# Optimization experiments

Measured on AMD Instinct MI355X. Metric: run time of the kernel, lower is better.

## Reference

```python
import jax, jax.numpy as jnp
import numpy as np

B, C, H, W = 4, 768, 64, 64
NC_PRED = 200   # classes in preds/text (!= 171 to trigger retrieval path)
NC_MEM = 171    # memory/text_coco classes
TC = 256        # transform_channels
OC = 768        # out_channels
BN_EPS = 1e-5


def setup_inputs() -> dict:
    key = jax.random.key(0)
    ks = jax.random.split(key, 32)
    n = lambda k, s, sc=1.0: jax.random.normal(k, s, jnp.float32) * sc
    g = lambda k, c: 1.0 + 0.1 * jax.random.normal(k, (c,), jnp.float32)
    inp = {
        'feats': n(ks[0], (B, C, H, W)),
        'preds': n(ks[1], (B, NC_PRED, H, W)),
        'text': n(ks[2], (1, NC_PRED, 1, C)),
        'memory': n(ks[3], (NC_MEM, 1, C)),      # self.memory buffer
        'text_mem': n(ks[4], (NC_MEM, 1, C)),    # self.text buffer
        # query_project: two 1x1 conv + BN + ReLU
        'qw1': n(ks[5], (TC, C), C ** -0.5), 'qg1': g(ks[6], TC), 'qb1': n(ks[7], (TC,), 0.1),
        'qw2': n(ks[8], (TC, TC), TC ** -0.5), 'qg2': g(ks[9], TC), 'qb2': n(ks[10], (TC,), 0.1),
        # key_project: two 1x1 conv + BN + ReLU
        'kw1': n(ks[11], (TC, C), C ** -0.5), 'kg1': g(ks[12], TC), 'kb1': n(ks[13], (TC,), 0.1),
        'kw2': n(ks[14], (TC, TC), TC ** -0.5), 'kg2': g(ks[15], TC), 'kb2': n(ks[16], (TC,), 0.1),
        # value_project: 1x1 conv + BN + ReLU
        'vw': n(ks[17], (TC, C), C ** -0.5), 'vg': g(ks[18], TC), 'vb': n(ks[19], (TC,), 0.1),
        # out_project: 1x1 conv + BN + ReLU (TC -> C)
        'ow': n(ks[20], (C, TC), TC ** -0.5), 'og': g(ks[21], C), 'ob': n(ks[22], (C,), 0.1),
        # bottleneck: 3x3 conv (2C -> OC) + BN + ReLU
        'bw': n(ks[23], (OC, 2 * C, 3, 3), (2 * C * 9) ** -0.5), 'bg': g(ks[24], OC), 'bb': n(ks[25], (OC,), 0.1),
    }
    return inp


def _cbr(x, w, gamma, beta):
    # 1x1 conv (no bias) + eval-mode BN (mean=0, var=1) + ReLU
    y = jnp.einsum('oc,bchw->bohw', w, x)
    s = (gamma / jnp.sqrt(1.0 + BN_EPS))[None, :, None, None]
    return jax.nn.relu(y * s + beta[None, :, None, None])


def _forward(feats, preds, text, memory, text_mem,
             qw1, qg1, qb1, qw2, qg2, qb2,
             kw1, kg1, kb1, kw2, kg2, kb2,
             vw, vg, vb, ow, og, ob, bw, bg, bb):
    b, c, h, w = feats.shape
    nc = preds.shape[1]
    # softmax class weights per pixel: [B*H*W, NC]
    wcls = jax.nn.softmax(preds.transpose(0, 2, 3, 1).reshape(-1, nc), axis=-1)
    # --- retrieval: cosine sim + argmax + gather (nc != 171 branch) ---
    t = text[0, :, 0, :]          # [NC_PRED, C]
    tc = text_mem[:, 0, :]        # [NC_MEM, C]
    mem = memory[:, 0, :]         # [NC_MEM, C]
    den = jnp.linalg.norm(t, axis=1)[:, None] * jnp.linalg.norm(tc, axis=1)[None, :]
    sim = (t @ tc.T) / jnp.maximum(den, 1e-8)
    idx = jnp.argmax(sim, axis=1)            # [NC_PRED]
    D = mem[idx]                             # gathered memory rows [NC_PRED, C]
    # soft aggregation
    sel = (wcls @ D).reshape(b, h, w, c).transpose(0, 3, 1, 2)  # [B,C,H,W]
    # --- self-attention: query=feats, key/value=selected memory ---
    q = _cbr(_cbr(feats, qw1, qg1, qb1), qw2, qg2, qb2).reshape(b, TC, h * w).transpose(0, 2, 1)  # [B,HW,TC]
    k = _cbr(_cbr(sel, kw1, kg1, kb1), kw2, kg2, kb2).reshape(b, TC, h * w)                        # [B,TC,HW]
    v = _cbr(sel, vw, vg, vb).reshape(b, TC, h * w).transpose(0, 2, 1)                             # [B,HW,TC]
    att = jax.nn.softmax(jnp.einsum('bqc,bck->bqk', q, k) * (TC ** -0.5), axis=-1)                 # [B,HW,HW]
    ctx = jnp.einsum('bqk,bkc->bqc', att, v).transpose(0, 2, 1).reshape(b, TC, h, w)
    sel_out = _cbr(ctx, ow, og, ob)          # [B,C,H,W]
    # --- bottleneck: 3x3 conv + BN + ReLU on concat ---
    x = jnp.concatenate([feats, sel_out], axis=1)
    y = jax.lax.conv_general_dilated(x, bw, (1, 1), 'SAME',
                                     dimension_numbers=('NCHW', 'OIHW', 'NCHW'))
    s = (bg / jnp.sqrt(1.0 + BN_EPS))[None, :, None, None]
    return jax.nn.relu(y * s + bb[None, :, None, None])


def reference(feats, preds, text, memory, text_mem,
              qw1, qg1, qb1, qw2, qg2, qb2,
              kw1, kg1, kb1, kw2, kg2, kb2,
              vw, vg, vb, ow, og, ob, bw, bg, bb):
    return _forward(feats, preds, text, memory, text_mem,
                    qw1, qg1, qb1, qw2, qg2, qb2,
                    kw1, kg1, kb1, kw2, kg2, kb2,
                    vw, vg, vb, ow, og, ob, bw, bg, bb)
```

## Files before the change

### kernel.cpp

```cpp
#include <hip/hip_runtime.h>
#include <stdint.h>

typedef unsigned short u16;
typedef __attribute__((ext_vector_type(8))) short short8;
typedef __attribute__((ext_vector_type(4))) float f32x4;

#define RSQC 0.9999950000374997f
#define OUT_ELEMS 12582912

__device__ __forceinline__ float bf2f(u16 u) {
  union { uint32_t i; float f; } v; v.i = ((uint32_t)u) << 16; return v.f;
}
__device__ __forceinline__ u16 f2bf(float f) {
  union { uint32_t i; float f; } v; v.f = f;
  uint32_t i = v.i;
  i += 0x7fffu + ((i >> 16) & 1u);
  return (u16)(i >> 16);
}

__global__ __launch_bounds__(256) void probe_fill(float* out, float val) {
  for (size_t i = (size_t)blockIdx.x * 256 + threadIdx.x; i < OUT_ELEMS; i += (size_t)gridDim.x * 256)
    out[i] = val;
}


__global__ __launch_bounds__(64) void sim_argmax(const float* __restrict__ text,
                                                 const float* __restrict__ tmem,
                                                 int* __restrict__ idx) {
  const int i = blockIdx.x, lane = threadIdx.x;
  const float* t = text + (size_t)i * 768;
  float nt = 0.f;
  for (int c = lane; c < 768; c += 64) { float x = t[c]; nt += x * x; }
#pragma unroll
  for (int m = 32; m; m >>= 1) nt += __shfl_xor(nt, m);
  nt = sqrtf(nt);
  float best = -1e30f; int bj = 0x7fffffff;
  for (int j = lane; j < 171; j += 64) {
    const float* tc = tmem + (size_t)j * 768;
    float dot = 0.f, nc = 0.f;
    for (int c = 0; c < 768; ++c) {
      float y = tc[c];
      dot += t[c] * y;
      nc += y * y;
    }
    float den = fmaxf(nt * sqrtf(nc), 1e-8f);
    float s = dot / den;
    if (s > best || (s == best && j < bj)) { best = s; bj = j; }
  }
#pragma unroll
  for (int m = 32; m; m >>= 1) {
    float ob = __shfl_xor(best, m); int oj = __shfl_xor(bj, m);
    if (ob > best || (ob == best && oj < bj)) { best = ob; bj = oj; }
  }
  if (lane == 0) idx[i] = bj;
}

__global__ __launch_bounds__(256) void build_d(const float* __restrict__ memory,
                                               const int* __restrict__ idx,
                                               u16* __restrict__ D) {
  int i = blockIdx.x * 256 + threadIdx.x;
  if (i >= 256 * 768) return;
  int c = i % 768, j = i / 768;
  u16 v = 0;
  if (j < 200) {
    int ii = idx[j];
    ii = ii < 0 ? 0 : (ii > 170 ? 170 : ii);
    v = f2bf(memory[(size_t)ii * 768 + c]);
  }
  D[i] = v;
}

__global__ __launch_bounds__(256) void wcls_kernel(const float* __restrict__ preds,
                                                   u16* __restrict__ wcls) {
  const int pos = blockIdx.x * 256 + threadIdx.x;
  const int b = pos >> 12, hw = pos & 4095;
  const float* p = preds + (size_t)b * 200 * 4096 + hw;
  float mx = -1e30f;
  for (int n = 0; n < 200; ++n) mx = fmaxf(mx, p[(size_t)n * 4096]);
  float s = 0.f;
  for (int n = 0; n < 200; ++n) s += __expf(p[(size_t)n * 4096] - mx);
  const float inv = 1.f / s;
  u16* w = wcls + (size_t)pos * 256;
  for (int nc = 0; nc < 32; ++nc) {
    short8 v;
#pragma unroll
    for (int j = 0; j < 8; ++j) {
      int n = nc * 8 + j;
      float e = (n < 200) ? __expf(p[(size_t)n * 4096] - mx) * inv : 0.f;
      v[j] = (short)f2bf(e);
    }
    *(short8*)&w[nc * 8] = v;
  }
}

__global__ __launch_bounds__(256) void transpose_feats(const float* __restrict__ feats,
                                                       u16* __restrict__ ft) {
  __shared__ u16 t[64][65];
  const int bz = blockIdx.z, c0 = blockIdx.y * 64, p0 = blockIdx.x * 64;
  const int col = threadIdx.x & 63, row4 = threadIdx.x >> 6;
  const float* src = feats + ((size_t)bz * 768 + c0) * 4096 + p0;
#pragma unroll
  for (int i = 0; i < 16; ++i) {
    int ci = i * 4 + row4;
    t[ci][col] = f2bf(src[(size_t)ci * 4096 + col]);
  }
  __syncthreads();
  u16* dst = ft + ((size_t)bz * 4096 + p0) * 768 + c0;
#pragma unroll
  for (int i = 0; i < 16; ++i) {
    int pi = i * 4 + row4;
    dst[(size_t)pi * 768 + col] = t[col][pi];
  }
}

__global__ __launch_bounds__(256) void cast_w(const float* __restrict__ src,
                                              u16* __restrict__ dst, int n) {
  int i = blockIdx.x * 256 + threadIdx.x;
  if (i < n) dst[i] = f2bf(src[i]);
}

__global__ __launch_bounds__(256) void repack_frag(const float* __restrict__ bw,
                                                   u16* __restrict__ w9f, int c_base) {
  size_t i = (size_t)blockIdx.x * 256 + threadIdx.x;
  if (i >= (size_t)5308416) return;
  int j = (int)(i & 7);
  int lane = (int)((i >> 3) & 63);
  int rem = (int)(i >> 9);
  int mfrag = rem % 48;
  int pt = rem / 48;
  int tap = pt % 9;
  int kc = pt / 9;
  int o = mfrag * 16 + (lane & 15);
  int c = kc * 32 + (lane >> 4) * 8 + j;
  w9f[i] = f2bf(bw[((size_t)o * 1536 + c_base + c) * 9 + tap]);
}


template <bool EP>
__global__ __launch_bounds__(256) void gemm_std(
    const u16* __restrict__ A, const u16* __restrict__ Bt, u16* __restrict__ out,
    const float* __restrict__ g, const float* __restrict__ bia,
    int N, int K, int lda, int ldb) {
  __shared__ __attribute__((aligned(16))) u16 As[2][128 * 32];
  __shared__ __attribute__((aligned(16))) u16 Bs[2][128 * 32];
  const int tid = threadIdx.x, lane = tid & 63, wv = tid >> 6;
  const int wr = wv >> 1, wc = wv & 1;
  const int m0 = blockIdx.y * 128, n0 = blockIdx.x * 128;
  const int r0 = lane >> 2, ksl = (lane & 3) * 8;
  const int wofs = (lane >> 2) * 32 + (((lane & 3) ^ ((lane >> 3) & 3)) << 3);
  const int rsl = (((lane >> 4) ^ ((lane >> 1) & 3)) << 3);
  f32x4 acc[4][4] = {};
  const int nt = K >> 5;

  short8 a0[2], b0[2], a1[2], b1[2];
  auto LOAD = [&](int t, short8 av[2], short8 bv[2]) {
    const int k0 = t << 5;
#pragma unroll
    for (int i = 0; i < 2; ++i) {
      const int row = (wv * 2 + i) * 16 + r0;
      av[i] = *(const short8*)(A + (size_t)(m0 + row) * lda + k0 + ksl);
      bv[i] = *(const short8*)(Bt + (size_t)(n0 + row) * ldb + k0 + ksl);
    }
  };
  auto STORE = [&](int buf, short8 av[2], short8 bv[2]) {
#pragma unroll
    for (int i = 0; i < 2; ++i) {
      const int o = (wv * 2 + i) * 512 + wofs;
      *(short8*)&As[buf][o] = av[i];
      *(short8*)&Bs[buf][o] = bv[i];
    }
  };
  auto COMPUTE = [&](int buf) {
    short8 a[4], b[4];
#pragma unroll
    for (int mi = 0; mi < 4; ++mi)
      a[mi] = *(const short8*)&As[buf][(wr * 4 + mi) * 512 + (lane & 15) * 32 + rsl];
#pragma unroll
    for (int ni = 0; ni < 4; ++ni)
      b[ni] = *(const short8*)&Bs[buf][(wc * 4 + ni) * 512 + (lane & 15) * 32 + rsl];
#pragma unroll
    for (int mi = 0; mi < 4; ++mi)
#pragma unroll
      for (int ni = 0; ni < 4; ++ni)
        acc[mi][ni] = __builtin_amdgcn_mfma_f32_16x16x32_bf16(a[mi], b[ni], acc[mi][ni], 0, 0, 0);
  };

  LOAD(0, a0, b0);
  for (int t = 0; t < nt; t += 2) {
    STORE(0, a0, b0);
    __syncthreads();
    LOAD(t + 1, a1, b1);
    COMPUTE(0);
    STORE(1, a1, b1);
    __syncthreads();
    if (t + 2 < nt) LOAD(t + 2, a0, b0);
    COMPUTE(1);
  }
  const int mb = m0 + wr * 64 + ((lane >> 4) << 2);
  const int nb = n0 + wc * 64 + (lane & 15);
#pragma unroll
  for (int ni = 0; ni < 4; ++ni) {
    const int n = nb + ni * 16;
    float s = 1.f, bb_ = 0.f;
    if (EP) { s = g[n] * RSQC; bb_ = bia[n]; }
#pragma unroll
    for (int mi = 0; mi < 4; ++mi)
#pragma unroll
      for (int r = 0; r < 4; ++r) {
        float v = acc[mi][ni][r];
        if (EP) v = fmaxf(v * s + bb_, 0.f);
        out[(size_t)(mb + mi * 16 + r) * N + n] = f2bf(v);
      }
  }
}

__global__ __launch_bounds__(256) void gemm_swv(
    const u16* __restrict__ A, const u16* __restrict__ Bt, u16* __restrict__ out,
    const float* __restrict__ g, const float* __restrict__ bia,
    int Mtot, int K, int lda, int ldb) {
  __shared__ __attribute__((aligned(16))) u16 As[2][128 * 32];
  __shared__ __attribute__((aligned(16))) u16 Bs[2][128 * 32];
  const int tid = threadIdx.x, lane = tid & 63, wv = tid >> 6;
  const int wr = wv >> 1, wc = wv & 1;
  const int m0 = blockIdx.y * 128, n0 = blockIdx.x * 128;
  const int r0 = lane >> 2, ksl = (lane & 3) * 8;
  const int wofs = (lane >> 2) * 32 + (((lane & 3) ^ ((lane >> 3) & 3)) << 3);
  const int rsl = (((lane >> 4) ^ ((lane >> 1) & 3)) << 3);
  f32x4 acc[4][4] = {};
  const int nt = K >> 5;

  short8 a0[2], b0[2], a1[2], b1[2];
  auto LOAD = [&](int t, short8 av[2], short8 bv[2]) {
    const int k0 = t << 5;
#pragma unroll
    for (int i = 0; i < 2; ++i) {
      const int row = (wv * 2 + i) * 16 + r0;
      av[i] = *(const short8*)(A + (size_t)(m0 + row) * lda + k0 + ksl);
      bv[i] = *(const short8*)(Bt + (size_t)(n0 + row) * ldb + k0 + ksl);
    }
  };
  auto STORE = [&](int buf, short8 av[2], short8 bv[2]) {
#pragma unroll
    for (int i = 0; i < 2; ++i) {
      const int o = (wv * 2 + i) * 512 + wofs;
      *(short8*)&As[buf][o] = av[i];
      *(short8*)&Bs[buf][o] = bv[i];
    }
  };
  auto COMPUTE = [&](int buf) {
    short8 a[4], b[4];
#pragma unroll
    for (int mi = 0; mi < 4; ++mi)
      a[mi] = *(const short8*)&As[buf][(wr * 4 + mi) * 512 + (lane & 15) * 32 + rsl];
#pragma unroll
    for (int ni = 0; ni < 4; ++ni)
      b[ni] = *(const short8*)&Bs[buf][(wc * 4 + ni) * 512 + (lane & 15) * 32 + rsl];
#pragma unroll
    for (int mi = 0; mi < 4; ++mi)
#pragma unroll
      for (int ni = 0; ni < 4; ++ni)
        acc[mi][ni] = __builtin_amdgcn_mfma_f32_16x16x32_bf16(a[mi], b[ni], acc[mi][ni], 0, 0, 0);
  };

  LOAD(0, a0, b0);
  for (int t = 0; t < nt; t += 2) {
    STORE(0, a0, b0);
    __syncthreads();
    LOAD(t + 1, a1, b1);
    COMPUTE(0);
    STORE(1, a1, b1);
    __syncthreads();
    if (t + 2 < nt) LOAD(t + 2, a0, b0);
    COMPUTE(1);
  }
  const int mb = m0 + wr * 64 + ((lane >> 4) << 2);
  const int nb = n0 + wc * 64 + (lane & 15);
#pragma unroll
  for (int mi = 0; mi < 4; ++mi)
#pragma unroll
    for (int r = 0; r < 4; ++r) {
      const int m = mb + mi * 16 + r;
      const float s = g[m] * RSQC, bb_ = bia[m];
#pragma unroll
      for (int ni = 0; ni < 4; ++ni) {
        const int n = nb + ni * 16;
        out[((size_t)(n >> 12) * Mtot + m) * 4096 + (n & 4095)] =
            f2bf(fmaxf(acc[mi][ni][r] * s + bb_, 0.f));
      }
    }
}

template <int MODE>
__global__ __launch_bounds__(256) void conv_frag(
    const u16* __restrict__ Af, const u16* __restrict__ X, float* out,
    const float* __restrict__ g, const float* __restrict__ bia) {
  __shared__ __attribute__((aligned(16))) u16 Hb[264 * 32];
  const int tid = threadIdx.x, lane = tid & 63, wv = tid >> 6;
  const int wr = wv >> 1, wc = wv & 1;
  const int id = blockIdx.y * 128 + blockIdx.x;
  const int xcd = id & 7, sl = id >> 3;
  const int m0 = (sl % 6) * 128;
  const int n0 = (xcd * 16 + sl / 6) * 128;
  f32x4 acc[4][4] = {};

  int vmask[4];
#pragma unroll
  for (int i = 0; i < 4; ++i) {
    const int hw = (n0 + wc * 64 + i * 16 + (lane & 15)) & 4095;
    const int h = hw >> 6, w = hw & 63;
    int m = 0;
#pragma unroll
    for (int t = 0; t < 9; ++t)
      if ((unsigned)(h + t / 3 - 1) < 64u && (unsigned)(w + t % 3 - 1) < 64u) m |= 1 << t;
    vmask[i] = m;
  }

  const int fb = (m0 >> 4) + wr * 4;
  auto aload = [&](int kc, int tap, short8 d[4]) {
    const u16* base = Af + ((size_t)((kc * 9 + tap) * 48 + fb) << 9) + lane * 8;
#pragma unroll
    for (int mi = 0; mi < 4; ++mi) d[mi] = *(const short8*)(base + (mi << 9));
  };

  short8 acur[4], anxt[4];
  aload(0, 0, acur);
  for (int kc = 0; kc < 24; ++kc) {
    short8 hreg[5];
#pragma unroll
    for (int j = 0; j < 5; ++j) {
      const int cid = tid + j * 256;
      if (cid < 1032) {
        int q = n0 - 65 + (cid >> 2);
        q = q < 0 ? 0 : (q > 16383 ? 16383 : q);
        hreg[j] = *(const short8*)(X + (size_t)q * 768 + kc * 32 + (cid & 3) * 8);
      }
    }
    __syncthreads();
#pragma unroll
    for (int j = 0; j < 5; ++j) {
      const int cid = tid + j * 256;
      if (cid < 1032) {
        const int s = cid & 3, row = cid >> 2;
        *(short8*)((char*)Hb + row * 64 + ((s ^ ((row >> 1) & 3)) << 4)) = hreg[j];
      }
    }
    __syncthreads();
#pragma unroll
    for (int tap = 0; tap < 9; ++tap) {
      const int nk = (tap == 8) ? (kc == 23 ? 23 : kc + 1) : kc;
      const int ntp = (tap == 8) ? 0 : tap + 1;
      aload(nk, ntp, anxt);
      const int shift = (tap / 3 - 1) * 64 + (tap % 3 - 1);
#pragma unroll
      for (int ni = 0; ni < 4; ++ni) {
        const int hrow = wc * 64 + ni * 16 + (lane & 15) + 65 + shift;
        short8 bv = *(const short8*)((const char*)Hb + hrow * 64 +
                                     (((lane >> 4) ^ ((hrow >> 1) & 3)) << 4));
        short8 z = {};
        if (!((vmask[ni] >> tap) & 1)) bv = z;
#pragma unroll
        for (int mi = 0; mi < 4; ++mi)
          acc[mi][ni] = __builtin_amdgcn_mfma_f32_16x16x32_bf16(acur[mi], bv, acc[mi][ni], 0, 0, 0);
      }
#pragma unroll
      for (int mi = 0; mi < 4; ++mi) acur[mi] = anxt[mi];
    }
  }
  const int mb = m0 + wr * 64 + ((lane >> 4) << 2);
  const int nb = n0 + wc * 64 + (lane & 15);
#pragma unroll
  for (int mi = 0; mi < 4; ++mi)
#pragma unroll
    for (int r = 0; r < 4; ++r) {
      const int m = mb + mi * 16 + r;
      float s = 0.f, bb_ = 0.f;
      if (MODE == 2) { s = g[m] * RSQC; bb_ = bia[m]; }
#pragma unroll
      for (int ni = 0; ni < 4; ++ni) {
        const int n = nb + ni * 16;
        const size_t oidx = ((size_t)(n >> 12) * 768 + m) * 4096 + (n & 4095);
        if (MODE == 1) out[oidx] = acc[mi][ni][r];
        else out[oidx] = fmaxf((acc[mi][ni][r] + out[oidx]) * s + bb_, 0.f);
      }
    }
}

__global__ __launch_bounds__(256) void flash_attn(const u16* Q,
                                                  const u16* __restrict__ Kg,
                                                  const u16* __restrict__ Vt,
                                                  u16* ctx) {
  __shared__ __attribute__((aligned(16))) u16 KVs[64 * 256];
  __shared__ __attribute__((aligned(16))) u16 Ps[4096];
  const int tid = threadIdx.x, lane = tid & 63, wv = tid >> 6;
  const int b = blockIdx.y, q0 = blockIdx.x * 64;
  const u16* qb = Q + ((size_t)b * 4096 + q0) * 256;
  const u16* kb = Kg + (size_t)b * 4096 * 256;
  const u16* vb = Vt + (size_t)b * 256 * 4096;
  const float scale = 0.0625f;

  short8 qf[8];
  {
    const int arow = wv * 16 + (lane & 15);
    const u16* qrow = qb + (size_t)arow * 256 + (lane >> 4) * 8;
#pragma unroll
    for (int kk = 0; kk < 8; ++kk) qf[kk] = *(const short8*)(qrow + kk * 32);
  }
  float mreg[4] = {-1e30f, -1e30f, -1e30f, -1e30f};
  float lsum[4] = {0.f, 0.f, 0.f, 0.f};
  f32x4 o[16] = {};

  for (int t = 0; t < 64; ++t) {
    {
      const int r = tid >> 5, sb = (tid & 31) * 16;
      const char* ksrc = (const char*)(kb + (size_t)t * 64 * 256);
#pragma unroll
      for (int i = 0; i < 8; ++i) {
        int row = i * 8 + r;
        short8 v = *(const short8*)(ksrc + (size_t)row * 512 + sb);
        *(short8*)((char*)KVs + row * 512 + (sb ^ ((row & 7) << 4))) = v;
      }
    }
    __syncthreads();
    f32x4 s4[4] = {};
    __builtin_amdgcn_s_setprio(1);
#pragma unroll
    for (int kk = 0; kk < 8; ++kk) {
      const int cb = (kk * 32 + ((lane >> 4) * 8)) * 2;
#pragma unroll
      for (int ni = 0; ni < 4; ++ni) {
        const int brow = ni * 16 + (lane & 15);
        short8 bb = *(const short8*)((const char*)KVs + brow * 512 + (cb ^ ((brow & 7) << 4)));
        s4[ni] = __builtin_amdgcn_mfma_f32_16x16x32_bf16(qf[kk], bb, s4[ni], 0, 0, 0);
      }
    }
    __builtin_amdgcn_s_setprio(0);
    float al[4], p[4][4];
#pragma unroll
    for (int r = 0; r < 4; ++r) {
      float v0 = fmaxf(fmaxf(s4[0][r], s4[1][r]), fmaxf(s4[2][r], s4[3][r]));
      v0 = fmaxf(v0, __shfl_xor(v0, 1));
      v0 = fmaxf(v0, __shfl_xor(v0, 2));
      v0 = fmaxf(v0, __shfl_xor(v0, 4));
      v0 = fmaxf(v0, __shfl_xor(v0, 8));
      const float mn = fmaxf(mreg[r], v0 * scale);
      al[r] = __expf(mreg[r] - mn);
      mreg[r] = mn;
      float srow = 0.f;
#pragma unroll
      for (int ni = 0; ni < 4; ++ni) {
        float pv = __expf(s4[ni][r] * scale - mn);
        p[ni][r] = pv;
        srow += pv;
      }
      srow += __shfl_xor(srow, 1);
      srow += __shfl_xor(srow, 2);
      srow += __shfl_xor(srow, 4);
      srow += __shfl_xor(srow, 8);
      lsum[r] = lsum[r] * al[r] + srow;
    }
#pragma unroll
    for (int nf = 0; nf < 16; ++nf)
#pragma unroll
      for (int r = 0; r < 4; ++r) o[nf][r] *= al[r];
    {
      char* pbase = (char*)Ps + wv * 2048;
#pragma unroll
      for (int ni = 0; ni < 4; ++ni)
#pragma unroll
        for (int r = 0; r < 4; ++r) {
          const int row = ((lane >> 4) << 2) + r, col = ni * 16 + (lane & 15);
          *(u16*)(pbase + row * 128 + ((col * 2) ^ ((row & 7) << 4))) = f2bf(p[ni][r]);
        }
    }
    __syncthreads();
    {
      const int slot = tid & 7;
#pragma unroll
      for (int i = 0; i < 8; ++i) {
        const int cc = i * 32 + (tid >> 3);
        short8 v = *(const short8*)((const char*)vb + ((size_t)cc * 4096 + t * 64) * 2 + slot * 16);
        *(short8*)((char*)KVs + cc * 128 + ((slot * 16) ^ ((cc & 7) << 4))) = v;
      }
    }
    __syncthreads();
    short8 pa[2];
#pragma unroll
    for (int kk = 0; kk < 2; ++kk) {
      const int row = lane & 15;
      const int cb = (kk * 32 + ((lane >> 4) * 8)) * 2;
      pa[kk] = *(const short8*)((const char*)Ps + wv * 2048 + row * 128 + (cb ^ ((row & 7) << 4)));
    }
    __builtin_amdgcn_s_setprio(1);
#pragma unroll
    for (int nf = 0; nf < 16; ++nf) {
      const int crow = nf * 16 + (lane & 15);
#pragma unroll
      for (int kk = 0; kk < 2; ++kk) {
        const int kb2 = (kk * 32 + ((lane >> 4) * 8)) * 2;
        short8 bb = *(const short8*)((const char*)KVs + crow * 128 + (kb2 ^ ((crow & 7) << 4)));
        o[nf] = __builtin_amdgcn_mfma_f32_16x16x32_bf16(pa[kk], bb, o[nf], 0, 0, 0);
      }
    }
    __builtin_amdgcn_s_setprio(0);
    __syncthreads();
  }
  u16* cb_ = ctx + ((size_t)b * 4096 + q0) * 256;
#pragma unroll
  for (int r = 0; r < 4; ++r) {
    const int row = wv * 16 + ((lane >> 4) << 2) + r;
    const float inv = 1.f / lsum[r];
#pragma unroll
    for (int nf = 0; nf < 16; ++nf) {
      const int col = nf * 16 + (lane & 15);
      cb_[(size_t)row * 256 + col] = f2bf(o[nf][r] * inv);
    }
  }
}


extern "C" void kernel_launch(void* const* d_in, const int* in_sizes, int n_in,
                              void* d_out, int out_size, void* d_ws, size_t ws_size,
                              hipStream_t stream) {
  (void)in_sizes; (void)n_in; (void)out_size;
  const float* feats  = (const float*)d_in[0];
  const float* preds  = (const float*)d_in[1];
  const float* text   = (const float*)d_in[2];
  const float* memory = (const float*)d_in[3];
  const float* tmem   = (const float*)d_in[4];
  const float* qw1 = (const float*)d_in[5];  const float* qg1 = (const float*)d_in[6];  const float* qb1 = (const float*)d_in[7];
  const float* qw2 = (const float*)d_in[8];  const float* qg2 = (const float*)d_in[9];  const float* qb2 = (const float*)d_in[10];
  const float* kw1 = (const float*)d_in[11]; const float* kg1 = (const float*)d_in[12]; const float* kb1 = (const float*)d_in[13];
  const float* kw2 = (const float*)d_in[14]; const float* kg2 = (const float*)d_in[15]; const float* kb2 = (const float*)d_in[16];
  const float* vw  = (const float*)d_in[17]; const float* vg  = (const float*)d_in[18]; const float* vb  = (const float*)d_in[19];
  const float* ow  = (const float*)d_in[20]; const float* og  = (const float*)d_in[21]; const float* ob  = (const float*)d_in[22];
  const float* bw  = (const float*)d_in[23]; const float* bg  = (const float*)d_in[24]; const float* bb  = (const float*)d_in[25];

  float* dout = (float*)d_out;
  char* ws = (char*)d_ws;
  u16* featsT = (u16*)(ws);
  u16* selout = (u16*)(ws + 25165824);
  u16* S2     = (u16*)(ws + 50331648);
  u16* qw1c   = (u16*)(ws + 58720256);
  u16* kw1c   = (u16*)(ws + 59113472);
  u16* vwc    = (u16*)(ws + 59506688);
  u16* owc    = (u16*)(ws + 59899904);
  u16* qw2c   = (u16*)(ws + 60293120);
  u16* kw2c   = (u16*)(ws + 60424192);
  u16* w9     = S2;
  const size_t WS_NEED = 60948480;
  u16* D   = selout;
  u16* KD  = (u16*)((char*)selout + 393216);
  u16* VD  = (u16*)((char*)selout + 524288);
  int* idx = (int*)((char*)selout + 655360);
  u16* O0 = (u16*)dout;
  u16* O1 = O0 + 4194304;
  u16* O2 = O0 + 8388608;

  if (ws_size < WS_NEED) {
    probe_fill<<<2048, 256, 0, stream>>>(dout, 1000.0f);
    return;
  }

  u16* wcls = O0;
  u16* k1 = S2, *q1 = S2;
  u16* kbuf = O1, *vT = O2;
  u16* qbuf = O0, *ctx = O0;

  sim_argmax<<<200, 64, 0, stream>>>(text, tmem, idx);
  build_d<<<768, 256, 0, stream>>>(memory, idx, D);
  wcls_kernel<<<64, 256, 0, stream>>>(preds, wcls);
  transpose_feats<<<dim3(64, 12, 4), 256, 0, stream>>>(feats, featsT);
  cast_w<<<768, 256, 0, stream>>>(qw1, qw1c, 196608);
  cast_w<<<768, 256, 0, stream>>>(kw1, kw1c, 196608);
  cast_w<<<768, 256, 0, stream>>>(vw, vwc, 196608);
  cast_w<<<768, 256, 0, stream>>>(ow, owc, 196608);
  cast_w<<<256, 256, 0, stream>>>(qw2, qw2c, 65536);
  cast_w<<<256, 256, 0, stream>>>(kw2, kw2c, 65536);

  gemm_std<false><<<dim3(2, 2), 256, 0, stream>>>(kw1c, D, KD, nullptr, nullptr, 256, 768, 768, 768);
  gemm_std<false><<<dim3(2, 2), 256, 0, stream>>>(vwc, D, VD, nullptr, nullptr, 256, 768, 768, 768);

  gemm_std<true><<<dim3(2, 128), 256, 0, stream>>>(wcls, KD, k1, kg1, kb1, 256, 256, 256, 256);
  gemm_std<true><<<dim3(2, 128), 256, 0, stream>>>(k1, kw2c, kbuf, kg2, kb2, 256, 256, 256, 256);
  gemm_swv<<<dim3(128, 2), 256, 0, stream>>>(VD, wcls, vT, vg, vb, 256, 256, 256, 256);
  gemm_std<true><<<dim3(2, 128), 256, 0, stream>>>(featsT, qw1c, q1, qg1, qb1, 256, 768, 768, 768);
  gemm_std<true><<<dim3(2, 128), 256, 0, stream>>>(q1, qw2c, qbuf, qg2, qb2, 256, 256, 256, 256);
  flash_attn<<<dim3(64, 4), 256, 0, stream>>>(qbuf, kbuf, vT, ctx);
  gemm_std<true><<<dim3(6, 128), 256, 0, stream>>>(ctx, owc, selout, og, ob, 768, 256, 256, 256);
  repack_frag<<<20736, 256, 0, stream>>>(bw, w9, 0);
  conv_frag<1><<<dim3(128, 6), 256, 0, stream>>>(w9, featsT, dout, nullptr, nullptr);
  repack_frag<<<20736, 256, 0, stream>>>(bw, w9, 768);
  conv_frag<2><<<dim3(128, 6), 256, 0, stream>>>(w9, selout, dout, bg, bb);
}
```

Before: 861.6 us.

## Double-buffer conv LDS tiles, parallelize softmax over classes, fuse weight casts

The conv kernel now uses two LDS halo buffers. It prefetches the next channel chunk into registers while computing the current one, leaving one barrier per iteration instead of two. The wcls softmax kernel spreads the 200 classes over 4 thread groups per pixel with a shared-memory reduction, and launches four times as many blocks to raise parallelism. Six weight-cast launches are merged into one kernel to cut launch overhead. LDS use in the conv doubles, which may reduce occupancy.

```diff
diff --git a/kernel.cpp b/kernel.cpp
--- a/kernel.cpp
+++ b/kernel.cpp
@@ -72,24 +72,36 @@
 
 __global__ __launch_bounds__(256) void wcls_kernel(const float* __restrict__ preds,
                                                    u16* __restrict__ wcls) {
-  const int pos = blockIdx.x * 256 + threadIdx.x;
+  __shared__ float red[4][64];
+  const int tid = threadIdx.x;
+  const int p = tid & 63, q = tid >> 6;
+  const int pos = blockIdx.x * 64 + p;
   const int b = pos >> 12, hw = pos & 4095;
-  const float* p = preds + (size_t)b * 200 * 4096 + hw;
+  const float* pp = preds + (size_t)b * 200 * 4096 + hw;
+  const int nlo = q * 50, nhi = nlo + 50;
   float mx = -1e30f;
-  for (int n = 0; n < 200; ++n) mx = fmaxf(mx, p[(size_t)n * 4096]);
+  for (int n = nlo; n < nhi; ++n) mx = fmaxf(mx, pp[(size_t)n * 4096]);
+  red[q][p] = mx;
+  __syncthreads();
+  const float m = fmaxf(fmaxf(red[0][p], red[1][p]), fmaxf(red[2][p], red[3][p]));
+  __syncthreads();
   float s = 0.f;
-  for (int n = 0; n < 200; ++n) s += __expf(p[(size_t)n * 4096] - mx);
-  const float inv = 1.f / s;
+  for (int n = nlo; n < nhi; ++n) s += __expf(pp[(size_t)n * 4096] - m);
+  red[q][p] = s;
+  __syncthreads();
+  const float inv = 1.f / (red[0][p] + red[1][p] + red[2][p] + red[3][p]);
   u16* w = wcls + (size_t)pos * 256;
-  for (int nc = 0; nc < 32; ++nc) {
+#pragma unroll
+  for (int c8 = 0; c8 < 8; ++c8) {
     short8 v;
+    const int base = q * 64 + c8 * 8;
 #pragma unroll
     for (int j = 0; j < 8; ++j) {
-      int n = nc * 8 + j;
-      float e = (n < 200) ? __expf(p[(size_t)n * 4096] - mx) * inv : 0.f;
+      const int n = base + j;
+      float e = (n < 200) ? __expf(pp[(size_t)n * 4096] - m) * inv : 0.f;
       v[j] = (short)f2bf(e);
     }
-    *(short8*)&w[nc * 8] = v;
+    *(short8*)&w[base] = v;
   }
 }
 
@@ -113,10 +125,20 @@
   }
 }
 
-__global__ __launch_bounds__(256) void cast_w(const float* __restrict__ src,
-                                              u16* __restrict__ dst, int n) {
+__global__ __launch_bounds__(256) void cast_all(
+    const float* __restrict__ s0, u16* __restrict__ d0,
+    const float* __restrict__ s1, u16* __restrict__ d1,
+    const float* __restrict__ s2, u16* __restrict__ d2,
+    const float* __restrict__ s3, u16* __restrict__ d3,
+    const float* __restrict__ s4, u16* __restrict__ d4,
+    const float* __restrict__ s5, u16* __restrict__ d5) {
   int i = blockIdx.x * 256 + threadIdx.x;
-  if (i < n) dst[i] = f2bf(src[i]);
+  if (i < 196608) d0[i] = f2bf(s0[i]);
+  else if (i < 393216) d1[i - 196608] = f2bf(s1[i - 196608]);
+  else if (i < 589824) d2[i - 393216] = f2bf(s2[i - 393216]);
+  else if (i < 786432) d3[i - 589824] = f2bf(s3[i - 589824]);
+  else if (i < 851968) d4[i - 786432] = f2bf(s4[i - 786432]);
+  else if (i < 917504) d5[i - 851968] = f2bf(s5[i - 851968]);
 }
 
 __global__ __launch_bounds__(256) void repack_frag(const float* __restrict__ bw,
@@ -294,7 +316,7 @@
 __global__ __launch_bounds__(256) void conv_frag(
     const u16* __restrict__ Af, const u16* __restrict__ X, float* out,
     const float* __restrict__ g, const float* __restrict__ bia) {
-  __shared__ __attribute__((aligned(16))) u16 Hb[264 * 32];
+  __shared__ __attribute__((aligned(16))) u16 Hb[2][264 * 32];
   const int tid = threadIdx.x, lane = tid & 63, wv = tid >> 6;
   const int wr = wv >> 1, wc = wv & 1;
   const int id = blockIdx.y * 128 + blockIdx.x;
@@ -321,11 +343,7 @@
 #pragma unroll
     for (int mi = 0; mi < 4; ++mi) d[mi] = *(const short8*)(base + (mi << 9));
   };
-
-  short8 acur[4], anxt[4];
-  aload(0, 0, acur);
-  for (int kc = 0; kc < 24; ++kc) {
-    short8 hreg[5];
+  auto hload = [&](int kc, short8 hreg[5]) {
 #pragma unroll
     for (int j = 0; j < 5; ++j) {
       const int cid = tid + j * 256;
@@ -335,16 +353,28 @@
         hreg[j] = *(const short8*)(X + (size_t)q * 768 + kc * 32 + (cid & 3) * 8);
       }
     }
-    __syncthreads();
+  };
+  auto hwrite = [&](int buf, short8 hreg[5]) {
 #pragma unroll
     for (int j = 0; j < 5; ++j) {
       const int cid = tid + j * 256;
       if (cid < 1032) {
         const int s = cid & 3, row = cid >> 2;
-        *(short8*)((char*)Hb + row * 64 + ((s ^ ((row >> 1) & 3)) << 4)) = hreg[j];
-      }
-    }
-    __syncthreads();
+        *(short8*)((char*)&Hb[buf][0] + row * 64 + ((s ^ ((row >> 1) & 3)) << 4)) = hreg[j];
+      }
+    }
+  };
+
+  short8 hreg[5];
+  hload(0, hreg);
+  hwrite(0, hreg);
+  __syncthreads();
+
+  short8 acur[4], anxt[4];
+  aload(0, 0, acur);
+  int p = 0;
+  for (int kc = 0; kc < 24; ++kc) {
+    if (kc < 23) hload(kc + 1, hreg);
 #pragma unroll
     for (int tap = 0; tap < 9; ++tap) {
       const int nk = (tap == 8) ? (kc == 23 ? 23 : kc + 1) : kc;
@@ -354,7 +384,7 @@
 #pragma unroll
       for (int ni = 0; ni < 4; ++ni) {
         const int hrow = wc * 64 + ni * 16 + (lane & 15) + 65 + shift;
-        short8 bv = *(const short8*)((const char*)Hb + hrow * 64 +
+        short8 bv = *(const short8*)((const char*)&Hb[p][0] + hrow * 64 +
                                      (((lane >> 4) ^ ((hrow >> 1) & 3)) << 4));
         short8 z = {};
         if (!((vmask[ni] >> tap) & 1)) bv = z;
@@ -364,6 +394,11 @@
       }
 #pragma unroll
       for (int mi = 0; mi < 4; ++mi) acur[mi] = anxt[mi];
+    }
+    if (kc < 23) {
+      hwrite(p ^ 1, hreg);
+      __syncthreads();
+      p ^= 1;
     }
   }
   const int mb = m0 + wr * 64 + ((lane >> 4) << 2);
@@ -568,14 +603,9 @@
 
   sim_argmax<<<200, 64, 0, stream>>>(text, tmem, idx);
   build_d<<<768, 256, 0, stream>>>(memory, idx, D);
-  wcls_kernel<<<64, 256, 0, stream>>>(preds, wcls);
+  wcls_kernel<<<256, 256, 0, stream>>>(preds, wcls);
   transpose_feats<<<dim3(64, 12, 4), 256, 0, stream>>>(feats, featsT);
-  cast_w<<<768, 256, 0, stream>>>(qw1, qw1c, 196608);
-  cast_w<<<768, 256, 0, stream>>>(kw1, kw1c, 196608);
-  cast_w<<<768, 256, 0, stream>>>(vw, vwc, 196608);
-  cast_w<<<768, 256, 0, stream>>>(ow, owc, 196608);
-  cast_w<<<256, 256, 0, stream>>>(qw2, qw2c, 65536);
-  cast_w<<<256, 256, 0, stream>>>(kw2, kw2c, 65536);
+  cast_all<<<3584, 256, 0, stream>>>(qw1, qw1c, kw1, kw1c, vw, vwc, ow, owc, qw2, qw2c, kw2, kw2c);
 
   gemm_std<false><<<dim3(2, 2), 256, 0, stream>>>(kw1c, D, KD, nullptr, nullptr, 256, 768, 768, 768);
   gemm_std<false><<<dim3(2, 2), 256, 0, stream>>>(vwc, D, VD, nullptr, nullptr, 256, 768, 768, 768);
```

Measured after the change: 815.4 us. -5.4%, faster.
